# Performance work log

Measured on AMD Instinct MI355X. Metric: run time of the kernel, lower is better.

Reference implementation:

```python
import jax, jax.numpy as jnp
import numpy as np

D_MODEL = 1024
N_HEAD = 16
D_FF = 4096
SEQ = 2048
BATCH = 4
EPS = 1e-5


def setup_inputs() -> dict:
    key = jax.random.key(0)
    ks = jax.random.split(key, 10)
    s = 0.02
    return {
        "src": jax.random.normal(ks[0], (SEQ, BATCH, D_MODEL), jnp.float32),
        "padding_mask": jnp.zeros((BATCH, SEQ), jnp.bool_),
        "w_qkv": jax.random.normal(ks[1], (3 * D_MODEL, D_MODEL), jnp.float32) * s,
        "fc_w": jax.random.normal(ks[2], (D_MODEL, D_MODEL), jnp.float32) * s,
        "fc_b": jnp.zeros((D_MODEL,), jnp.float32),
        "w1": jax.random.normal(ks[3], (D_FF, D_MODEL), jnp.float32) * s,
        "b1": jnp.zeros((D_FF,), jnp.float32),
        "w2": jax.random.normal(ks[4], (D_MODEL, D_FF), jnp.float32) * s,
        "b2": jnp.zeros((D_MODEL,), jnp.float32),
        "g1": jnp.ones((D_MODEL,), jnp.float32),
        "be1": jnp.zeros((D_MODEL,), jnp.float32),
        "g2": jnp.ones((D_MODEL,), jnp.float32),
        "be2": jnp.zeros((D_MODEL,), jnp.float32),
    }


def _layer_norm(x, g, b):
    mu = jnp.mean(x, axis=-1, keepdims=True)
    var = jnp.mean(jnp.square(x - mu), axis=-1, keepdims=True)
    return (x - mu) * jax.lax.rsqrt(var + EPS) * g + b


def _mha(src, padding_mask, w_qkv, fc_w, fc_b):
    L, B, D = src.shape
    H = N_HEAD
    dh = D // H
    qkv = jnp.einsum("lbd,ed->lbe", src, w_qkv)  # (L,B,3D)
    q, k, v = jnp.split(qkv, 3, axis=-1)
    # (L, B*H, dh) -> (B*H, L, dh)
    q = q.reshape(L, B * H, dh).transpose(1, 0, 2)
    k = k.reshape(L, B * H, dh).transpose(1, 0, 2)
    v = v.reshape(L, B * H, dh).transpose(1, 0, 2)
    scores = jnp.einsum("nqd,nkd->nqk", q, k) / np.sqrt(dh).astype(np.float32)
    scores = scores.reshape(B, H, L, L)
    scores = jnp.where(padding_mask[:, None, None, :], -jnp.inf, scores)
    attn = jax.nn.softmax(scores, axis=-1).reshape(B * H, L, L)
    out = jnp.einsum("nqk,nkd->nqd", attn, v)  # (B*H, L, dh)
    out = out.transpose(1, 0, 2).reshape(L, B, D)
    return out @ fc_w.T + fc_b


def reference(src, padding_mask, w_qkv, fc_w, fc_b, w1, b1, w2, b2, g1, be1, g2, be2):
    src2 = _mha(src, padding_mask, w_qkv, fc_w, fc_b)
    src = _layer_norm(src + src2, g1, be1)
    h = jax.nn.relu(src @ w1.T + b1)
    src2 = h @ w2.T + b2
    return _layer_norm(src + src2, g2, be2)
```

## Files before the change

kernel.cpp:

```cpp
#include <hip/hip_runtime.h>
#include <cstdint>
#include <cstddef>

typedef __attribute__((ext_vector_type(8))) short bf16x8;
typedef __attribute__((ext_vector_type(4))) float f32x4;
typedef __attribute__((ext_vector_type(16))) float f32x16;

static __device__ __forceinline__ unsigned short f2bf(float f) {
    union { float f; unsigned u; } v; v.f = f;
    unsigned r = v.u + 0x7FFFu + ((v.u >> 16) & 1u);
    return (unsigned short)(r >> 16);
}
static __device__ __forceinline__ float bf2f(unsigned short u) {
    union { unsigned u; float f; } v; v.u = ((unsigned)u) << 16; return v.f;
}

static __device__ __forceinline__ void gld_lds16(const void* g, void* l) {
    unsigned loff = (unsigned)(size_t)l;
    loff = (unsigned)__builtin_amdgcn_readfirstlane((int)loff);
    __builtin_amdgcn_global_load_lds(
        (const __attribute__((address_space(1))) unsigned int*)(size_t)g,
        (__attribute__((address_space(3))) unsigned int*)(size_t)loff,
        16, 0, 0);
}

__global__ __launch_bounds__(256) void k_cvt5(
    const float* __restrict__ p0, const float* __restrict__ p1,
    const float* __restrict__ p2, const float* __restrict__ p3,
    const float* __restrict__ p4,
    unsigned short* __restrict__ q0, unsigned short* __restrict__ q1,
    unsigned short* __restrict__ q2, unsigned short* __restrict__ q3,
    unsigned short* __restrict__ q4)
{
    const int blk = blockIdx.x;
    const float* in; unsigned short* out; int base;
    if      (blk < 3072)  { in = p0; out = q0; base = blk; }
    else if (blk < 4096)  { in = p1; out = q1; base = blk - 3072; }
    else if (blk < 8192)  { in = p2; out = q2; base = blk - 4096; }
    else if (blk < 12288) { in = p3; out = q3; base = blk - 8192; }
    else                  { in = p4; out = q4; base = blk - 12288; }
    const int i = (base * 256 + threadIdx.x) * 4;
    float4 v = *reinterpret_cast<const float4*>(in + i);
    ushort4 o;
    o.x = f2bf(v.x); o.y = f2bf(v.y); o.z = f2bf(v.z); o.w = f2bf(v.w);
    *reinterpret_cast<ushort4*>(out + i) = o;
}

template<int BM, int MF>
__global__ __launch_bounds__(512, 2) void k_gemm8(
    const unsigned short* __restrict__ A, const unsigned short* __restrict__ W,
    float* __restrict__ Cf, unsigned short* __restrict__ Cb,
    const float* __restrict__ bias,
    int M, int N, int K, int scale_cols, float scale, int relu)
{
    __shared__ unsigned short As[2][BM * 64];
    __shared__ unsigned short Bs[2][256 * 64];
    const int tid = threadIdx.x, wid = tid >> 6, lane = tid & 63;
    const int lr = lane & 15, g16 = (lane >> 4) * 16;
    const int wm = wid >> 2, wn = wid & 3;

    const int nbx = N >> 8;
    const int nwg = gridDim.x;
    const int raw = blockIdx.x;
    const int swz = (raw & 7) * (nwg >> 3) + (raw >> 3);
    const int bm = (swz / nbx) * BM, bn = (swz % nbx) * 256;

    const int rin = tid >> 3;
    const int cole = (((tid & 7) * 16) ^ ((rin & 7) << 4)) >> 1;

    auto STAGE = [&](int bb, int kt1) {
        #pragma unroll
        for (int c = 0; c < BM / 64; ++c)
            gld_lds16(A + (size_t)(bm + c * 64 + rin) * K + kt1 + cole,
                      (char*)As[bb] + c * 8192 + wid * 1024);
        #pragma unroll
        for (int c = 0; c < 4; ++c)
            gld_lds16(W + (size_t)(bn + c * 64 + rin) * K + kt1 + cole,
                      (char*)Bs[bb] + c * 8192 + wid * 1024);
    };

    f32x4 acc[MF][4] = {};

    STAGE(0, 0);
    STAGE(1, 64);
    int cur = 0;

    for (int kt = 0; kt < K; kt += 64) {
        if (kt + 64 < K) {
            if constexpr (BM == 256) asm volatile("s_waitcnt vmcnt(8)" ::: "memory");
            else                     asm volatile("s_waitcnt vmcnt(6)" ::: "memory");
        } else {
            asm volatile("s_waitcnt vmcnt(0)" ::: "memory");
        }
        __builtin_amdgcn_s_barrier();

        const char* Ab = (const char*)As[cur];
        const char* Bb = (const char*)Bs[cur];
        bf16x8 bfr[4][2];

        #pragma unroll
        for (int p = 0; p < MF / 2; ++p) {
            bf16x8 af[2][2];
            #pragma unroll
            for (int mi = 0; mi < 2; ++mi)
                #pragma unroll
                for (int kk = 0; kk < 2; ++kk) {
                    const int row = wm * (MF * 16) + (2 * p + mi) * 16 + lr;
                    af[mi][kk] = *reinterpret_cast<const bf16x8*>(
                        Ab + row * 128 + ((kk * 64 + g16) ^ ((row & 7) << 4)));
                }
            if (p == 0) {
                #pragma unroll
                for (int n = 0; n < 4; ++n)
                    #pragma unroll
                    for (int kk = 0; kk < 2; ++kk) {
                        const int row = wn * 64 + n * 16 + lr;
                        bfr[n][kk] = *reinterpret_cast<const bf16x8*>(
                            Bb + row * 128 + ((kk * 64 + g16) ^ ((row & 7) << 4)));
                    }
            }
            __builtin_amdgcn_s_barrier();
            __builtin_amdgcn_s_setprio(1);
            #pragma unroll
            for (int mi = 0; mi < 2; ++mi)
                #pragma unroll
                for (int n = 0; n < 4; ++n)
                    #pragma unroll
                    for (int kk = 0; kk < 2; ++kk)
                        acc[2 * p + mi][n] = __builtin_amdgcn_mfma_f32_16x16x32_bf16(
                            af[mi][kk], bfr[n][kk], acc[2 * p + mi][n], 0, 0, 0);
            __builtin_amdgcn_s_setprio(0);
            __builtin_amdgcn_s_barrier();
        }
        if (kt + 128 < K) STAGE(cur, kt + 128);
        cur ^= 1;
    }

    #pragma unroll
    for (int m = 0; m < MF; ++m) {
        #pragma unroll
        for (int n = 0; n < 4; ++n) {
            const int col = bn + wn * 64 + n * 16 + lr;
            const float bv = bias ? bias[col] : 0.0f;
            const float sc = (col < scale_cols) ? scale : 1.0f;
            #pragma unroll
            for (int r = 0; r < 4; ++r) {
                const int row = bm + wm * (MF * 16) + m * 16 + (lane >> 4) * 4 + r;
                float v = acc[m][n][r] * sc + bv;
                if (relu) v = fmaxf(v, 0.0f);
                if (Cb) Cb[(size_t)row * N + col] = f2bf(v);
                else    Cf[(size_t)row * N + col] = v;
            }
        }
    }
}

__global__ __launch_bounds__(256) void k_vtrans(
    const unsigned short* __restrict__ qkv, unsigned short* __restrict__ vt)
{
    __shared__ unsigned short T[64][72];
    const int n = blockIdx.y, b = n >> 4, h = n & 15;
    const int l0 = blockIdx.x * 64;
    const int tid = threadIdx.x;
    {
        const int l = tid >> 2, d = (tid & 3) * 16;
        const unsigned short* p = qkv + (size_t)(l0 + l) * 12288 + b * 3072 + 2048 + h * 64 + d;
        *reinterpret_cast<bf16x8*>(&T[l][d])     = *reinterpret_cast<const bf16x8*>(p);
        *reinterpret_cast<bf16x8*>(&T[l][d + 8]) = *reinterpret_cast<const bf16x8*>(p + 8);
    }
    __syncthreads();
    {
        const int d = tid >> 2, lc = (tid & 3) * 16;
        unsigned short tmp[16];
        #pragma unroll
        for (int j = 0; j < 16; ++j) tmp[j] = T[lc + j][d];
        unsigned short* q = vt + ((size_t)n * 64 + d) * 2048 + l0 + lc;
        *reinterpret_cast<bf16x8*>(q)     = *reinterpret_cast<bf16x8*>(tmp);
        *reinterpret_cast<bf16x8*>(q + 8) = *reinterpret_cast<bf16x8*>(tmp + 8);
    }
}

__global__ __launch_bounds__(512) void k_attn(
    const unsigned short* __restrict__ qkv,
    const unsigned short* __restrict__ vt,
    const unsigned char* __restrict__ mask,
    unsigned short* __restrict__ out)
{
    __shared__ unsigned short Ks[2][64 * 64];
    __shared__ unsigned short Vs[2][64 * 64];
    const int tid = threadIdx.x, wid = tid >> 6, lane = tid & 63;
    const int q32 = lane & 31, hi = lane >> 5;
    const int raw = blockIdx.x;
    const int swz = (raw & 7) * 32 + (raw >> 3);
    const int n = swz >> 2, qblk = swz & 3;
    const int b = n >> 4, h = n & 15;
    const int qbase = qblk * 512 + wid * 64;
    const size_t SL = 12288;

    bf16x8 qfa[4], qfb[4];
    {
        const unsigned short* qra = qkv + (size_t)(qbase + q32) * SL + (size_t)b * 3072 + h * 64;
        const unsigned short* qrb = qra + 32 * SL;
        #pragma unroll
        for (int t = 0; t < 4; ++t) {
            qfa[t] = *reinterpret_cast<const bf16x8*>(qra + t * 16 + hi * 8);
            qfb[t] = *reinterpret_cast<const bf16x8*>(qrb + t * 16 + hi * 8);
        }
    }

    bool anym;
    {
        const uint4* mp = reinterpret_cast<const uint4*>(mask + b * 2048);
        uint4 m0 = mp[lane * 2], m1 = mp[lane * 2 + 1];
        unsigned mo = m0.x | m0.y | m0.z | m0.w | m1.x | m1.y | m1.z | m1.w;
        anym = __any(mo != 0);
    }

    const int sw = (q32 & 7) << 4;
    int koff[4], voff[2][2];
    #pragma unroll
    for (int t = 0; t < 4; ++t) koff[t] = q32 * 128 + ((t * 32 + hi * 16) ^ sw);
    #pragma unroll
    for (int ks = 0; ks < 2; ++ks)
        #pragma unroll
        for (int hf = 0; hf < 2; ++hf)
            voff[ks][hf] = q32 * 128 + ((ks * 64 + hf * 32 + hi * 16) ^ sw);

    const int soff = wid * 1024 + lane * 16;
    const int srow = soff >> 7;
    const int sbc  = (soff & 127) ^ ((srow & 7) << 4);
    const unsigned short* kgbase = qkv + (size_t)b * 3072 + 1024 + h * 64;
    const unsigned short* vgbase = vt + (size_t)n * 64 * 2048;

    #define STAGE(buf, kt)                                                            \
        do {                                                                          \
            gld_lds16(kgbase + (size_t)((kt) + srow) * SL + (sbc >> 1),               \
                      (char*)Ks[buf] + wid * 1024);                                   \
            gld_lds16(vgbase + (size_t)srow * 2048 + (kt) + (sbc >> 1),               \
                      (char*)Vs[buf] + wid * 1024);                                   \
        } while (0)

    f32x16 o0a = {}, o1a = {}, o2a = {};
    f32x16 o0b = {}, o1b = {}, o2b = {};
    union { unsigned w[4]; bf16x8 v; } onesf;
    onesf.w[0] = 0x3F803F80u; onesf.w[1] = 0x3F803F80u;
    onesf.w[2] = 0x3F803F80u; onesf.w[3] = 0x3F803F80u;

    STAGE(0, 0);
    int cur = 0;

    for (int kt = 0; kt < 2048; kt += 64) {
        __syncthreads();
        if (kt + 64 < 2048) STAGE(cur ^ 1, kt + 64);
        const char* Kb = (const char*)Ks[cur];
        const char* Vb = (const char*)Vs[cur];

        #pragma unroll
        for (int ks = 0; ks < 2; ++ks) {
            bf16x8 kf0 = *reinterpret_cast<const bf16x8*>(Kb + ks * 4096 + koff[0]);
            bf16x8 kf1 = *reinterpret_cast<const bf16x8*>(Kb + ks * 4096 + koff[1]);
            bf16x8 kf2 = *reinterpret_cast<const bf16x8*>(Kb + ks * 4096 + koff[2]);
            bf16x8 kf3 = *reinterpret_cast<const bf16x8*>(Kb + ks * 4096 + koff[3]);
            f32x16 sa = {}, sb = {};
            __builtin_amdgcn_s_setprio(1);
            sa = __builtin_amdgcn_mfma_f32_32x32x16_bf16(kf0, qfa[0], sa, 0, 0, 0);
            sb = __builtin_amdgcn_mfma_f32_32x32x16_bf16(kf0, qfb[0], sb, 0, 0, 0);
            sa = __builtin_amdgcn_mfma_f32_32x32x16_bf16(kf1, qfa[1], sa, 0, 0, 0);
            sb = __builtin_amdgcn_mfma_f32_32x32x16_bf16(kf1, qfb[1], sb, 0, 0, 0);
            sa = __builtin_amdgcn_mfma_f32_32x32x16_bf16(kf2, qfa[2], sa, 0, 0, 0);
            sb = __builtin_amdgcn_mfma_f32_32x32x16_bf16(kf2, qfb[2], sb, 0, 0, 0);
            sa = __builtin_amdgcn_mfma_f32_32x32x16_bf16(kf3, qfa[3], sa, 0, 0, 0);
            sb = __builtin_amdgcn_mfma_f32_32x32x16_bf16(kf3, qfb[3], sb, 0, 0, 0);
            __builtin_amdgcn_s_setprio(0);

            if (anym) {
                #pragma unroll
                for (int r = 0; r < 16; ++r) {
                    const int kl = (r & 3) + 8 * (r >> 2) + 4 * hi;
                    if (mask[b * 2048 + kt + ks * 32 + kl]) { sa[r] = -3e8f; sb[r] = -3e8f; }
                }
            }

            #pragma unroll
            for (int i = 0; i < 16; ++i) sa[i] = __builtin_amdgcn_exp2f(sa[i]);
            #pragma unroll
            for (int i = 0; i < 16; ++i) sb[i] = __builtin_amdgcn_exp2f(sb[i]);

            unsigned pka[8], pkb[8];
            #pragma unroll
            for (int i = 0; i < 8; ++i) {
                asm("v_cvt_pk_bf16_f32 %0, %1, %2" : "=v"(pka[i]) : "v"(sa[2 * i]), "v"(sa[2 * i + 1]));
                asm("v_cvt_pk_bf16_f32 %0, %1, %2" : "=v"(pkb[i]) : "v"(sb[2 * i]), "v"(sb[2 * i + 1]));
            }
            asm("v_permlane32_swap_b32 %0, %1" : "+v"(pka[2]), "+v"(pka[0]));
            asm("v_permlane32_swap_b32 %0, %1" : "+v"(pka[3]), "+v"(pka[1]));
            asm("v_permlane32_swap_b32 %0, %1" : "+v"(pka[6]), "+v"(pka[4]));
            asm("v_permlane32_swap_b32 %0, %1" : "+v"(pka[7]), "+v"(pka[5]));
            asm("v_permlane32_swap_b32 %0, %1" : "+v"(pkb[2]), "+v"(pkb[0]));
            asm("v_permlane32_swap_b32 %0, %1" : "+v"(pkb[3]), "+v"(pkb[1]));
            asm("v_permlane32_swap_b32 %0, %1" : "+v"(pkb[6]), "+v"(pkb[4]));
            asm("v_permlane32_swap_b32 %0, %1" : "+v"(pkb[7]), "+v"(pkb[5]));
            union { unsigned w[4]; bf16x8 v; } pa0, pa1, pb0, pb1;
            pa0.w[0] = pka[0]; pa0.w[1] = pka[1]; pa0.w[2] = pka[2]; pa0.w[3] = pka[3];
            pa1.w[0] = pka[4]; pa1.w[1] = pka[5]; pa1.w[2] = pka[6]; pa1.w[3] = pka[7];
            pb0.w[0] = pkb[0]; pb0.w[1] = pkb[1]; pb0.w[2] = pkb[2]; pb0.w[3] = pkb[3];
            pb1.w[0] = pkb[4]; pb1.w[1] = pkb[5]; pb1.w[2] = pkb[6]; pb1.w[3] = pkb[7];

            const bf16x8 v00 = *reinterpret_cast<const bf16x8*>(Vb + voff[ks][0]);
            const bf16x8 v01 = *reinterpret_cast<const bf16x8*>(Vb + voff[ks][1]);
            const bf16x8 v10 = *reinterpret_cast<const bf16x8*>(Vb + 4096 + voff[ks][0]);
            const bf16x8 v11 = *reinterpret_cast<const bf16x8*>(Vb + 4096 + voff[ks][1]);
            __builtin_amdgcn_s_setprio(1);
            o0a = __builtin_amdgcn_mfma_f32_32x32x16_bf16(v00, pa0.v, o0a, 0, 0, 0);
            o0b = __builtin_amdgcn_mfma_f32_32x32x16_bf16(v00, pb0.v, o0b, 0, 0, 0);
            o0a = __builtin_amdgcn_mfma_f32_32x32x16_bf16(v01, pa1.v, o0a, 0, 0, 0);
            o0b = __builtin_amdgcn_mfma_f32_32x32x16_bf16(v01, pb1.v, o0b, 0, 0, 0);
            o1a = __builtin_amdgcn_mfma_f32_32x32x16_bf16(v10, pa0.v, o1a, 0, 0, 0);
            o1b = __builtin_amdgcn_mfma_f32_32x32x16_bf16(v10, pb0.v, o1b, 0, 0, 0);
            o1a = __builtin_amdgcn_mfma_f32_32x32x16_bf16(v11, pa1.v, o1a, 0, 0, 0);
            o1b = __builtin_amdgcn_mfma_f32_32x32x16_bf16(v11, pb1.v, o1b, 0, 0, 0);
            o2a = __builtin_amdgcn_mfma_f32_32x32x16_bf16(onesf.v, pa0.v, o2a, 0, 0, 0);
            o2b = __builtin_amdgcn_mfma_f32_32x32x16_bf16(onesf.v, pb0.v, o2b, 0, 0, 0);
            o2a = __builtin_amdgcn_mfma_f32_32x32x16_bf16(onesf.v, pa1.v, o2a, 0, 0, 0);
            o2b = __builtin_amdgcn_mfma_f32_32x32x16_bf16(onesf.v, pb1.v, o2b, 0, 0, 0);
            __builtin_amdgcn_s_setprio(0);
        }
        cur ^= 1;
    }
    #undef STAGE

    const float rla = 1.0f / o2a[0];
    const float rlb = 1.0f / o2b[0];
    unsigned short* orowa = out + ((size_t)(qbase + q32) * 4 + b) * 1024 + h * 64;
    unsigned short* orowb = orowa + (size_t)32 * 4096;
    #pragma unroll
    for (int q4 = 0; q4 < 4; ++q4) {
        unsigned w0, w1, w2, w3;
        asm("v_cvt_pk_bf16_f32 %0, %1, %2" : "=v"(w0) : "v"(o0a[q4 * 4 + 0] * rla), "v"(o0a[q4 * 4 + 1] * rla));
        asm("v_cvt_pk_bf16_f32 %0, %1, %2" : "=v"(w1) : "v"(o0a[q4 * 4 + 2] * rla), "v"(o0a[q4 * 4 + 3] * rla));
        asm("v_cvt_pk_bf16_f32 %0, %1, %2" : "=v"(w2) : "v"(o1a[q4 * 4 + 0] * rla), "v"(o1a[q4 * 4 + 1] * rla));
        asm("v_cvt_pk_bf16_f32 %0, %1, %2" : "=v"(w3) : "v"(o1a[q4 * 4 + 2] * rla), "v"(o1a[q4 * 4 + 3] * rla));
        uint2 ua; ua.x = w0; ua.y = w1;
        uint2 ub; ub.x = w2; ub.y = w3;
        *reinterpret_cast<uint2*>(orowa + q4 * 8 + hi * 4)      = ua;
        *reinterpret_cast<uint2*>(orowa + 32 + q4 * 8 + hi * 4) = ub;
        asm("v_cvt_pk_bf16_f32 %0, %1, %2" : "=v"(w0) : "v"(o0b[q4 * 4 + 0] * rlb), "v"(o0b[q4 * 4 + 1] * rlb));
        asm("v_cvt_pk_bf16_f32 %0, %1, %2" : "=v"(w1) : "v"(o0b[q4 * 4 + 2] * rlb), "v"(o0b[q4 * 4 + 3] * rlb));
        asm("v_cvt_pk_bf16_f32 %0, %1, %2" : "=v"(w2) : "v"(o1b[q4 * 4 + 0] * rlb), "v"(o1b[q4 * 4 + 1] * rlb));
        asm("v_cvt_pk_bf16_f32 %0, %1, %2" : "=v"(w3) : "v"(o1b[q4 * 4 + 2] * rlb), "v"(o1b[q4 * 4 + 3] * rlb));
        uint2 uc; uc.x = w0; uc.y = w1;
        uint2 ud; ud.x = w2; ud.y = w3;
        *reinterpret_cast<uint2*>(orowb + q4 * 8 + hi * 4)      = uc;
        *reinterpret_cast<uint2*>(orowb + 32 + q4 * 8 + hi * 4) = ud;
    }
}

template<int OUTF>
__global__ __launch_bounds__(256) void k_add_ln(
    const unsigned short* __restrict__ x, const unsigned short* __restrict__ y,
    const float* __restrict__ gamma, const float* __restrict__ beta,
    float* __restrict__ outf, unsigned short* __restrict__ outb)
{
    const int row = blockIdx.x * 4 + (threadIdx.x >> 6);
    const int lane = threadIdx.x & 63;
    const size_t base = (size_t)row * 1024;
    float v[16];
    float s = 0.0f, ss = 0.0f;
    #pragma unroll
    for (int i = 0; i < 4; ++i) {
        const int c = lane * 4 + i * 256;
        ushort4 a = *reinterpret_cast<const ushort4*>(x + base + c);
        ushort4 d = *reinterpret_cast<const ushort4*>(y + base + c);
        v[i * 4 + 0] = bf2f(a.x) + bf2f(d.x); v[i * 4 + 1] = bf2f(a.y) + bf2f(d.y);
        v[i * 4 + 2] = bf2f(a.z) + bf2f(d.z); v[i * 4 + 3] = bf2f(a.w) + bf2f(d.w);
        #pragma unroll
        for (int j = 0; j < 4; ++j) { s += v[i * 4 + j]; ss += v[i * 4 + j] * v[i * 4 + j]; }
    }
    #pragma unroll
    for (int o = 1; o < 64; o <<= 1) { s += __shfl_xor(s, o); ss += __shfl_xor(ss, o); }
    const float mu = s * (1.0f / 1024.0f);
    const float var = ss * (1.0f / 1024.0f) - mu * mu;
    const float rstd = rsqrtf(var + 1e-5f);
    #pragma unroll
    for (int i = 0; i < 4; ++i) {
        const int c = lane * 4 + i * 256;
        float4 gq = *reinterpret_cast<const float4*>(gamma + c);
        float4 bq = *reinterpret_cast<const float4*>(beta + c);
        float o0 = (v[i * 4 + 0] - mu) * rstd * gq.x + bq.x;
        float o1 = (v[i * 4 + 1] - mu) * rstd * gq.y + bq.y;
        float o2 = (v[i * 4 + 2] - mu) * rstd * gq.z + bq.z;
        float o3 = (v[i * 4 + 3] - mu) * rstd * gq.w + bq.w;
        if (OUTF) {
            float4 o; o.x = o0; o.y = o1; o.z = o2; o.w = o3;
            *reinterpret_cast<float4*>(outf + base + c) = o;
        } else {
            ushort4 ob;
            ob.x = f2bf(o0); ob.y = f2bf(o1); ob.z = f2bf(o2); ob.w = f2bf(o3);
            *reinterpret_cast<ushort4*>(outb + base + c) = ob;
        }
    }
}

extern "C" void kernel_launch(void* const* d_in, const int* in_sizes, int n_in,
                              void* d_out, int out_size, void* d_ws, size_t ws_size,
                              hipStream_t stream) {
    const float* src  = (const float*)d_in[0];
    const unsigned char* mask = (const unsigned char*)d_in[1];
    const float* w_qkv = (const float*)d_in[2];
    const float* fc_w = (const float*)d_in[3];
    const float* fc_b = (const float*)d_in[4];
    const float* w1   = (const float*)d_in[5];
    const float* b1   = (const float*)d_in[6];
    const float* w2   = (const float*)d_in[7];
    const float* b2   = (const float*)d_in[8];
    const float* g1   = (const float*)d_in[9];
    const float* be1  = (const float*)d_in[10];
    const float* g2   = (const float*)d_in[11];
    const float* be2  = (const float*)d_in[12];
    float* out = (float*)d_out;

    char* ws = (char*)d_ws;
    size_t o = 0;
    auto take = [&](size_t nbytes) { size_t p = o; o += (nbytes + 255) & ~(size_t)255; return p; };
    unsigned short* wqkv_b = (unsigned short*)(ws + take((size_t)3072 * 1024 * 2));
    unsigned short* fcw_b  = (unsigned short*)(ws + take((size_t)1024 * 1024 * 2));
    unsigned short* w1_b   = (unsigned short*)(ws + take((size_t)4096 * 1024 * 2));
    unsigned short* w2_b   = (unsigned short*)(ws + take((size_t)1024 * 4096 * 2));
    unsigned short* src_b  = (unsigned short*)(ws + take((size_t)8192 * 1024 * 2));
    unsigned short* qkv_b  = (unsigned short*)(ws + take((size_t)8192 * 3072 * 2));
    unsigned short* attn_b = (unsigned short*)(ws + take((size_t)8192 * 1024 * 2));
    unsigned short* h_b    = (unsigned short*)(ws + take((size_t)8192 * 4096 * 2));
    unsigned short* proj_b = qkv_b;
    unsigned short* y_b    = qkv_b;
    unsigned short* x1_b   = src_b;
    unsigned short* vt_b   = h_b;

    k_cvt5<<<dim3(20480), 256, 0, stream>>>(w_qkv, fc_w, w1, w2, src,
                                            wqkv_b, fcw_b, w1_b, w2_b, src_b);

    k_gemm8<256, 8><<<dim3((8192 / 256) * (3072 / 256)), 512, 0, stream>>>(
        src_b, wqkv_b, nullptr, qkv_b, nullptr, 8192, 3072, 1024, 1024, 0.18033688011112042f, 0);

    k_vtrans<<<dim3(32, 64), 256, 0, stream>>>(qkv_b, vt_b);

    k_attn<<<dim3(256), 512, 0, stream>>>(qkv_b, vt_b, mask, attn_b);

    k_gemm8<128, 4><<<dim3((8192 / 128) * (1024 / 256)), 512, 0, stream>>>(
        attn_b, fcw_b, nullptr, proj_b, fc_b, 8192, 1024, 1024, 0, 1.0f, 0);

    k_add_ln<0><<<dim3(8192 / 4), 256, 0, stream>>>(src_b, proj_b, g1, be1, nullptr, x1_b);

    k_gemm8<256, 8><<<dim3((8192 / 256) * (4096 / 256)), 512, 0, stream>>>(
        x1_b, w1_b, nullptr, h_b, b1, 8192, 4096, 1024, 0, 1.0f, 1);

    k_gemm8<128, 4><<<dim3((8192 / 128) * (1024 / 256)), 512, 0, stream>>>(
        h_b, w2_b, nullptr, y_b, b2, 8192, 1024, 4096, 0, 1.0f, 0);

    k_add_ln<1><<<dim3(8192 / 4), 256, 0, stream>>>(x1_b, y_b, g2, be2, out, nullptr);
}
```

Before: 394.2 us.

## Use split-K with 256-row tiles for N=1024 GEMMs, reduce partials in add+LayerNorm

The two N=1024 GEMMs (output projection and FFN down-projection) move from 128x256 tiles to 256x256 tiles with a two-way split along K. This keeps the same 256-block grid while raising per-block data reuse. Each split writes a bf16 partial into a separate buffer. The add+LayerNorm kernel now sums both partials plus the bias, so the reduction and bias are fused there. The cost is extra partial-buffer traffic and rounding each partial to bf16 before summing, which may slightly reduce accuracy.

```diff
diff --git a/kernel.cpp b/kernel.cpp
--- a/kernel.cpp
+++ b/kernel.cpp
@@ -46,7 +46,7 @@
     *reinterpret_cast<ushort4*>(out + i) = o;
 }
 
-template<int BM, int MF>
+template<int BM, int MF, int KS>
 __global__ __launch_bounds__(512, 2) void k_gemm8(
     const unsigned short* __restrict__ A, const unsigned short* __restrict__ W,
     float* __restrict__ Cf, unsigned short* __restrict__ Cb,
@@ -63,7 +63,11 @@
     const int nwg = gridDim.x;
     const int raw = blockIdx.x;
     const int swz = (raw & 7) * (nwg >> 3) + (raw >> 3);
-    const int bm = (swz / nbx) * BM, bn = (swz % nbx) * 256;
+    const int base_grid = nwg / KS;
+    const int sid = (KS > 1) ? (swz / base_grid) : 0;
+    const int tile = (KS > 1) ? (swz % base_grid) : swz;
+    const int bm = (tile / nbx) * BM, bn = (tile % nbx) * 256;
+    const int kbeg = sid * (K / KS), kend = kbeg + K / KS;
 
     const int rin = tid >> 3;
     const int cole = (((tid & 7) * 16) ^ ((rin & 7) << 4)) >> 1;
@@ -81,12 +85,12 @@
 
     f32x4 acc[MF][4] = {};
 
-    STAGE(0, 0);
-    STAGE(1, 64);
+    STAGE(0, kbeg);
+    STAGE(1, kbeg + 64);
     int cur = 0;
 
-    for (int kt = 0; kt < K; kt += 64) {
-        if (kt + 64 < K) {
+    for (int kt = kbeg; kt < kend; kt += 64) {
+        if (kt + 64 < kend) {
             if constexpr (BM == 256) asm volatile("s_waitcnt vmcnt(8)" ::: "memory");
             else                     asm volatile("s_waitcnt vmcnt(6)" ::: "memory");
         } else {
@@ -132,10 +136,11 @@
             __builtin_amdgcn_s_setprio(0);
             __builtin_amdgcn_s_barrier();
         }
-        if (kt + 128 < K) STAGE(cur, kt + 128);
+        if (kt + 128 < kend) STAGE(cur, kt + 128);
         cur ^= 1;
     }
 
+    unsigned short* Cbp = Cb ? Cb + (size_t)sid * M * N : nullptr;
     #pragma unroll
     for (int m = 0; m < MF; ++m) {
         #pragma unroll
@@ -148,8 +153,8 @@
                 const int row = bm + wm * (MF * 16) + m * 16 + (lane >> 4) * 4 + r;
                 float v = acc[m][n][r] * sc + bv;
                 if (relu) v = fmaxf(v, 0.0f);
-                if (Cb) Cb[(size_t)row * N + col] = f2bf(v);
-                else    Cf[(size_t)row * N + col] = v;
+                if (Cbp) Cbp[(size_t)row * N + col] = f2bf(v);
+                else     Cf[(size_t)row * N + col] = v;
             }
         }
     }
@@ -356,8 +361,10 @@
 }
 
 template<int OUTF>
-__global__ __launch_bounds__(256) void k_add_ln(
-    const unsigned short* __restrict__ x, const unsigned short* __restrict__ y,
+__global__ __launch_bounds__(256) void k_add_ln3(
+    const unsigned short* __restrict__ x,
+    const unsigned short* __restrict__ y0, const unsigned short* __restrict__ y1,
+    const float* __restrict__ bias,
     const float* __restrict__ gamma, const float* __restrict__ beta,
     float* __restrict__ outf, unsigned short* __restrict__ outb)
 {
@@ -369,10 +376,14 @@
     #pragma unroll
     for (int i = 0; i < 4; ++i) {
         const int c = lane * 4 + i * 256;
-        ushort4 a = *reinterpret_cast<const ushort4*>(x + base + c);
-        ushort4 d = *reinterpret_cast<const ushort4*>(y + base + c);
-        v[i * 4 + 0] = bf2f(a.x) + bf2f(d.x); v[i * 4 + 1] = bf2f(a.y) + bf2f(d.y);
-        v[i * 4 + 2] = bf2f(a.z) + bf2f(d.z); v[i * 4 + 3] = bf2f(a.w) + bf2f(d.w);
+        ushort4 a  = *reinterpret_cast<const ushort4*>(x + base + c);
+        ushort4 d0 = *reinterpret_cast<const ushort4*>(y0 + base + c);
+        ushort4 d1 = *reinterpret_cast<const ushort4*>(y1 + base + c);
+        float4 bb  = *reinterpret_cast<const float4*>(bias + c);
+        v[i * 4 + 0] = bf2f(a.x) + bf2f(d0.x) + bf2f(d1.x) + bb.x;
+        v[i * 4 + 1] = bf2f(a.y) + bf2f(d0.y) + bf2f(d1.y) + bb.y;
+        v[i * 4 + 2] = bf2f(a.z) + bf2f(d0.z) + bf2f(d1.z) + bb.z;
+        v[i * 4 + 3] = bf2f(a.w) + bf2f(d0.w) + bf2f(d1.w) + bb.w;
         #pragma unroll
         for (int j = 0; j < 4; ++j) { s += v[i * 4 + j]; ss += v[i * 4 + j] * v[i * 4 + j]; }
     }
@@ -430,31 +441,32 @@
     unsigned short* qkv_b  = (unsigned short*)(ws + take((size_t)8192 * 3072 * 2));
     unsigned short* attn_b = (unsigned short*)(ws + take((size_t)8192 * 1024 * 2));
     unsigned short* h_b    = (unsigned short*)(ws + take((size_t)8192 * 4096 * 2));
-    unsigned short* proj_b = qkv_b;
-    unsigned short* y_b    = qkv_b;
+    unsigned short* part_b = qkv_b;
     unsigned short* x1_b   = src_b;
     unsigned short* vt_b   = h_b;
 
     k_cvt5<<<dim3(20480), 256, 0, stream>>>(w_qkv, fc_w, w1, w2, src,
                                             wqkv_b, fcw_b, w1_b, w2_b, src_b);
 
-    k_gemm8<256, 8><<<dim3((8192 / 256) * (3072 / 256)), 512, 0, stream>>>(
+    k_gemm8<256, 8, 1><<<dim3((8192 / 256) * (3072 / 256)), 512, 0, stream>>>(
         src_b, wqkv_b, nullptr, qkv_b, nullptr, 8192, 3072, 1024, 1024, 0.18033688011112042f, 0);
 
     k_vtrans<<<dim3(32, 64), 256, 0, stream>>>(qkv_b, vt_b);
 
     k_attn<<<dim3(256), 512, 0, stream>>>(qkv_b, vt_b, mask, attn_b);
 
-    k_gemm8<128, 4><<<dim3((8192 / 128) * (1024 / 256)), 512, 0, stream>>>(
-        attn_b, fcw_b, nullptr, proj_b, fc_b, 8192, 1024, 1024, 0, 1.0f, 0);
-
-    k_add_ln<0><<<dim3(8192 / 4), 256, 0, stream>>>(src_b, proj_b, g1, be1, nullptr, x1_b);
-
-    k_gemm8<256, 8><<<dim3((8192 / 256) * (4096 / 256)), 512, 0, stream>>>(
+    k_gemm8<256, 8, 2><<<dim3((8192 / 256) * (1024 / 256) * 2), 512, 0, stream>>>(
+        attn_b, fcw_b, nullptr, part_b, nullptr, 8192, 1024, 1024, 0, 1.0f, 0);
+
+    k_add_ln3<0><<<dim3(8192 / 4), 256, 0, stream>>>(
+        src_b, part_b, part_b + (size_t)8192 * 1024, fc_b, g1, be1, nullptr, x1_b);
+
+    k_gemm8<256, 8, 1><<<dim3((8192 / 256) * (4096 / 256)), 512, 0, stream>>>(
         x1_b, w1_b, nullptr, h_b, b1, 8192, 4096, 1024, 0, 1.0f, 1);
 
-    k_gemm8<128, 4><<<dim3((8192 / 128) * (1024 / 256)), 512, 0, stream>>>(
-        h_b, w2_b, nullptr, y_b, b2, 8192, 1024, 4096, 0, 1.0f, 0);
-
-    k_add_ln<1><<<dim3(8192 / 4), 256, 0, stream>>>(x1_b, y_b, g2, be2, out, nullptr);
-}
+    k_gemm8<256, 8, 2><<<dim3((8192 / 256) * (1024 / 256) * 2), 512, 0, stream>>>(
+        h_b, w2_b, nullptr, part_b, nullptr, 8192, 1024, 4096, 0, 1.0f, 0);
+
+    k_add_ln3<1><<<dim3(8192 / 4), 256, 0, stream>>>(
+        x1_b, part_b, part_b + (size_t)8192 * 1024, b2, g2, be2, out, nullptr);
+}
```

Result: no change. 396.8 us (+0.6%).
